# Performance work log

Hardware: AMD Instinct MI355X
Metric: run time of the kernel (lower is better)

## Reference

```python
import jax, jax.numpy as jnp
import numpy as np

B, L, D_IN, H, N, NL = 16, 5000, 12, 256, 32, 4  # N = d_state//2 complex modes


def layer_norm(x, g, b, eps=1e-5):
    m = x.mean(-1, keepdims=True)
    v = ((x - m) ** 2).mean(-1, keepdims=True)
    return (x - m) * jax.lax.rsqrt(v + eps) * g + b


def s4d_kernel(log_dt, logA_re, A_im, Cp, length):
    # S4D-style diagonal SSM kernel (ZOH discretization), conjugate-symmetric -> 2*real
    dt = jnp.exp(log_dt)                      # (H,)
    A = -jnp.exp(logA_re) + 1j * A_im         # (H, N)
    C = Cp[..., 0] + 1j * Cp[..., 1]          # (H, N)
    dtA = A * dt[:, None]                     # (H, N)
    Ct = C * (jnp.exp(dtA) - 1.0) / A         # (H, N)
    V = jnp.exp(dtA[:, :, None] * jnp.arange(length, dtype=log_dt.dtype))  # (H, N, L) Vandermonde
    return 2.0 * jnp.einsum('hn,hnl->hl', Ct, V).real  # (H, L)


def s4_block(u, log_dt, logA_re, A_im, Cp, D, W_glu, b_glu):
    # u: (B, L, H), transposed=False convention
    length = u.shape[1]
    K = s4d_kernel(log_dt, logA_re, A_im, Cp, length)     # (H, L)
    n_fft = 2 * length
    k_f = jnp.fft.rfft(K, n=n_fft)                        # (H, F)
    u_f = jnp.fft.rfft(u, n=n_fft, axis=1)                # (B, F, H)
    y = jnp.fft.irfft(u_f * k_f.T[None], n=n_fft, axis=1)[:, :length]  # causal conv
    y = y + u * D                                         # skip connection
    y = jax.nn.gelu(y)
    y = y @ W_glu + b_glu                                 # (B, L, 2H)
    return jax.nn.glu(y, axis=-1)                         # (B, L, H)


def setup_inputs() -> dict:
    key = jax.random.key(0)
    ks = jax.random.split(key, 8)
    dt_min, dt_max = 1e-3, 1e-1
    log_dt = np.log(dt_min) + jax.random.uniform(ks[2], (NL, H)) * (np.log(dt_max) - np.log(dt_min))
    A_im = jnp.broadcast_to(np.pi * jnp.arange(N, dtype=jnp.float32), (NL, H, N)).copy()
    return {
        'x': jax.random.normal(ks[0], (B, L, D_IN), jnp.float32),
        'W_in': jax.random.normal(ks[1], (D_IN, H), jnp.float32) / np.sqrt(D_IN),
        'b_in': jnp.zeros((H,), jnp.float32),
        'ln_g': jnp.ones((NL, H), jnp.float32),
        'ln_b': jnp.zeros((NL, H), jnp.float32),
        'log_dt': log_dt.astype(jnp.float32),
        'logA_re': jnp.full((NL, H, N), np.log(0.5), jnp.float32),
        'A_im': A_im,
        'Cp': jax.random.normal(ks[3], (NL, H, N, 2), jnp.float32) * (0.5 ** 0.5),
        'D': jax.random.normal(ks[4], (NL, H), jnp.float32),
        'W_glu': jax.random.normal(ks[5], (NL, H, 2 * H), jnp.float32) / np.sqrt(H),
        'b_glu': jnp.zeros((NL, 2 * H), jnp.float32),
        'fn_g': jnp.ones((H,), jnp.float32),
        'fn_b': jnp.zeros((H,), jnp.float32),
    }


def reference(x, W_in, b_in, ln_g, ln_b, log_dt, logA_re, A_im, Cp, D, W_glu, b_glu, fn_g, fn_b):
    x = x @ W_in + b_in  # (B, L, H)
    for i in range(NL):
        z = layer_norm(x, ln_g[i], ln_b[i])  # prenorm
        residual = z
        y = s4_block(z, log_dt[i], logA_re[i], A_im[i], Cp[i], D[i], W_glu[i], b_glu[i])
        x = y + residual  # dropout is identity in eval
    return layer_norm(x, fn_g, fn_b)
```

## Files before the change

### kernel.cpp

```cpp
#include <hip/hip_runtime.h>
#include <math.h>

#define BB 16
#define LL 5000
#define DIN 12
#define HH 256
#define NN 32
#define NLAYER 4
#define LC 128
#define NCH 40
#define TAIL 8
#define COLS (BB*NCH)
#define NROWS (BB*LL)
#define KU 192

typedef __attribute__((ext_vector_type(8))) _Float16 f16x8;
typedef __attribute__((ext_vector_type(4))) float f32x4;

__device__ __forceinline__ float fast_gelu(float a) {
  float z = fmaf(0.0713548163f * a, a * a, 1.5957691216f * a);
  float e = __expf(-z);
  return a * __builtin_amdgcn_rcpf(1.0f + e);
}

__device__ __forceinline__ unsigned pk2h(float a, float b) {
  union { _Float16 h[2]; unsigned u; } x;
  x.h[0] = (_Float16)a; x.h[1] = (_Float16)b;
  return x.u;
}

__device__ __forceinline__ float2 upk2(unsigned u) {
  union { unsigned u; _Float16 h[2]; } x;
  x.u = u;
  return make_float2((float)x.h[0], (float)x.h[1]);
}

__global__ __launch_bounds__(128) void paramT_kernel(
    const float* __restrict__ log_dt, const float* __restrict__ logA_re,
    const float* __restrict__ A_im, const float* __restrict__ Cp,
    const float* __restrict__ Dv, int l,
    _Float16* __restrict__ Tc, _Float16* __restrict__ V, float* __restrict__ WLc) {
  int h = blockIdx.x;
  int t = threadIdx.x;
  __shared__ float s_are[NN], s_aim[NN], s_cre[NN], s_cim[NN];
  __shared__ float s_K[128];
  if (t < NN) {
    int n = t;
    int idx = (l * HH + h) * NN + n;
    float dt = expf(log_dt[l * HH + h]);
    float Are = -expf(logA_re[idx]);
    float Aim = A_im[idx];
    float are = Are * dt, aim = Aim * dt;
    float e = expf(are);
    float wre = e * cosf(aim), wim = e * sinf(aim);
    float cr = Cp[2 * idx], ci = Cp[2 * idx + 1];
    float nre = wre - 1.0f, nim = wim;
    float tre = cr * nre - ci * nim;
    float tim = cr * nim + ci * nre;
    float inv = 1.0f / (Are * Are + Aim * Aim);
    s_are[n] = are; s_aim[n] = aim;
    s_cre[n] = 2.0f * (tre * Are + tim * Aim) * inv;
    s_cim[n] = 2.0f * (tim * Are - tre * Aim) * inv;
    float eL = expf(128.0f * are);
    float ang = 128.0f * aim;
    WLc[h * 64 + 2 * n] = eL * cosf(ang);
    WLc[h * 64 + 2 * n + 1] = eL * sinf(ang);
  }
  __syncthreads();
  {
    float ksum = 0.0f;
    unsigned* brow = (unsigned*)(Tc + ((size_t)h * 128 + t) * KU + 128);
    for (int n = 0; n < NN; n++) {
      float are = s_are[n], aim = s_aim[n];
      float cre = s_cre[n], cim = s_cim[n];
      float ft = (float)t;
      float E = expf(are * ft);
      float a = aim * ft;
      float wtre = E * cosf(a), wtim = E * sinf(a);
      ksum = fmaf(cre, wtre, ksum);
      ksum = fmaf(-cim, wtim, ksum);
      float ew = expf(are);
      float wre = ew * cosf(aim), wim = ew * sinf(aim);
      float wpre = wtre * wre - wtim * wim;
      float wpim = wtre * wim + wtim * wre;
      float bre = cre * wpre - cim * wpim;
      float bim = -(cre * wpim + cim * wpre);
      brow[n] = pk2h(bre, bim);
      float fk = (float)(127 - t);
      float E2 = expf(are * fk);
      float a2 = aim * fk;
      V[((size_t)h * 64 + 2 * n) * 128 + t] = (_Float16)(E2 * cosf(a2));
      V[((size_t)h * 64 + 2 * n + 1) * 128 + t] = (_Float16)(E2 * sinf(a2));
    }
    s_K[t] = ksum;
  }
  __syncthreads();
  float D = Dv[l * HH + h];
  unsigned* row = (unsigned*)(Tc + ((size_t)h * 128 + t) * KU);
  for (int q = 0; q < 64; q++) {
    float v0 = 0.0f, v1 = 0.0f;
    int d0 = t - 2 * q;
    int d1 = d0 - 1;
    if (d0 >= 0) v0 = s_K[d0] + (d0 == 0 ? D : 0.0f);
    if (d1 >= 0) v1 = s_K[d1] + (d1 == 0 ? D : 0.0f);
    row[q] = pk2h(v0, v1);
  }
}

__global__ __launch_bounds__(256) void wt_kernel(
    const float* __restrict__ W, _Float16* __restrict__ Wt) {
  int gid = blockIdx.x * 256 + threadIdx.x;
  int l = gid >> 9, col = gid & 511;
  const float* w = W + (size_t)l * HH * 512 + col;
  _Float16* o = Wt + (size_t)gid * HH;
  for (int k = 0; k < HH; k++) o[k] = (_Float16)(w[(size_t)k * 512]);
}

__global__ __launch_bounds__(256) void proj_kernel(
    const float* __restrict__ x, const float* __restrict__ Win,
    const float* __restrict__ bin, _Float16* __restrict__ X) {
  int tp = threadIdx.x & 127, rs = threadIdx.x >> 7;
  int h0 = 2 * tp;
  float w0[DIN], w1[DIN];
#pragma unroll
  for (int k = 0; k < DIN; k++) {
    w0[k] = Win[k * HH + h0];
    w1[k] = Win[k * HH + h0 + 1];
  }
  float b0 = bin[h0], b1 = bin[h0 + 1];
  for (int row = blockIdx.x * 2 + rs; row < NROWS; row += gridDim.x * 2) {
    float a0 = b0, a1 = b1;
#pragma unroll
    for (int k = 0; k < DIN; k++) {
      float xv = x[(size_t)row * DIN + k];
      a0 = fmaf(xv, w0[k], a0);
      a1 = fmaf(xv, w1[k], a1);
    }
    *(unsigned*)(X + (size_t)row * HH + h0) = pk2h(a0, a1);
  }
}

__global__ __launch_bounds__(256) void ln_kernel(
    const _Float16* __restrict__ in, float* __restrict__ out,
    const float* __restrict__ g, const float* __restrict__ b) {
  int wave = threadIdx.x >> 6, lane = threadIdx.x & 63;
  int row = blockIdx.x * 4 + wave;
  uint2 pv = *(const uint2*)(in + (size_t)row * HH + 4 * lane);
  float2 v01 = upk2(pv.x), v23 = upk2(pv.y);
  float s = v01.x + v01.y + v23.x + v23.y;
  float q = v01.x * v01.x + v01.y * v01.y + v23.x * v23.x + v23.y * v23.y;
#pragma unroll
  for (int m = 1; m < 64; m <<= 1) { s += __shfl_xor(s, m); q += __shfl_xor(q, m); }
  float mean = s * (1.0f / HH);
  float var = q * (1.0f / HH) - mean * mean;
  float rstd = rsqrtf(var + 1e-5f);
  float4 gg = ((const float4*)g)[lane];
  float4 bb = ((const float4*)b)[lane];
  float4 o;
  o.x = (v01.x - mean) * rstd * gg.x + bb.x;
  o.y = (v01.y - mean) * rstd * gg.y + bb.y;
  o.z = (v23.x - mean) * rstd * gg.z + bb.z;
  o.w = (v23.y - mean) * rstd * gg.w + bb.w;
  ((float4*)(out + (size_t)row * HH))[lane] = o;
}

__global__ __launch_bounds__(256) void lnU_kernel(
    _Float16* __restrict__ stream, _Float16* __restrict__ U,
    const float* __restrict__ g, const float* __restrict__ b) {
  __shared__ unsigned short Ut[64][260];
  int col = blockIdx.x;
  int bI = col / NCH, cI = col % NCH;
  int len = (cI == NCH - 1) ? TAIL : 128;
  int wave = threadIdx.x >> 6, lane = threadIdx.x & 63;
  float4 gg = ((const float4*)g)[lane];
  float4 bv = ((const float4*)b)[lane];
  size_t base = ((size_t)bI * LL + (size_t)cI * 128) * HH;
#pragma unroll
  for (int half = 0; half < 2; half++) {
    if (half) __syncthreads();
    int t0 = half * 64;
    int lenh = len - t0;
    lenh = lenh < 0 ? 0 : (lenh > 64 ? 64 : lenh);
    for (int idx = threadIdx.x; idx < (64 - lenh) * 260; idx += 256) {
      int r = idx / 260;
      Ut[lenh + r][idx - r * 260] = 0;
    }
    for (int it = 0; it < 16; it++) {
      int tl = it * 4 + wave;
      if (tl < lenh) {
        int tau = t0 + tl;
        uint2 pv = *(const uint2*)(stream + base + (size_t)tau * HH + 4 * lane);
        float2 v01 = upk2(pv.x), v23 = upk2(pv.y);
        float s = v01.x + v01.y + v23.x + v23.y;
        float q = v01.x * v01.x + v01.y * v01.y + v23.x * v23.x + v23.y * v23.y;
#pragma unroll
        for (int m = 1; m < 64; m <<= 1) { s += __shfl_xor(s, m); q += __shfl_xor(q, m); }
        float mean = s * (1.0f / HH);
        float var = q * (1.0f / HH) - mean * mean;
        float rstd = rsqrtf(var + 1e-5f);
        float o0 = (v01.x - mean) * rstd * gg.x + bv.x;
        float o1 = (v01.y - mean) * rstd * gg.y + bv.y;
        float o2 = (v23.x - mean) * rstd * gg.z + bv.z;
        float o3 = (v23.y - mean) * rstd * gg.w + bv.w;
        uint2 p;
        p.x = pk2h(o0, o1);
        p.y = pk2h(o2, o3);
        *(uint2*)(stream + base + (size_t)tau * HH + 4 * lane) = p;
        *(uint2*)&Ut[tl][4 * lane] = p;
      }
    }
    __syncthreads();
    for (int rep = 0; rep < 8; rep++) {
      int linear = rep * 256 + threadIdx.x;
      int h = linear >> 3, ub = linear & 7;
      unsigned* dst = (unsigned*)(U + ((size_t)h * COLS + col) * KU) + half * 32;
#pragma unroll
      for (int s2 = 0; s2 < 4; s2++) {
        int u = ub + s2 * 8;
        dst[u] = (unsigned)Ut[2 * u][h] | ((unsigned)Ut[2 * u + 1][h] << 16);
      }
    }
  }
}

__global__ __launch_bounds__(256) void gemmA_kernel(
    const _Float16* __restrict__ V, const _Float16* __restrict__ U,
    _Float16* __restrict__ P) {
  __shared__ _Float16 As[64 * 72];
  __shared__ _Float16 Bs[128 * 72];
  int h = blockIdx.x, c0 = blockIdx.y * 128;
  int t = threadIdx.x;
  int w = t >> 6, lane = t & 63, lr = lane & 15, quad = lane >> 4;
  int mh = w & 1, nh = w >> 1;
  f32x4 acc[2][4];
#pragma unroll
  for (int i = 0; i < 2; i++)
#pragma unroll
    for (int j = 0; j < 4; j++) acc[i][j] = (f32x4)(0.0f);

  for (int kt = 0; kt < 128; kt += 64) {
#pragma unroll
    for (int i = 0; i < 2; i++) {
      int idx = t + 256 * i;
      int m = idx >> 3, q = idx & 7;
      *(uint4*)&As[m * 72 + q * 8] =
          *(const uint4*)(V + ((size_t)h * 64 + m) * 128 + kt + q * 8);
    }
#pragma unroll
    for (int i = 0; i < 4; i++) {
      int idx = t + 256 * i;
      int jj = idx >> 3, q = idx & 7;
      *(uint4*)&Bs[jj * 72 + q * 8] =
          *(const uint4*)(U + ((size_t)h * COLS + c0 + jj) * KU + kt + q * 8);
    }
    __syncthreads();
#pragma unroll
    for (int ks = 0; ks < 2; ks++) {
      f16x8 af[2], bf[4];
#pragma unroll
      for (int i = 0; i < 2; i++)
        af[i] = *(const f16x8*)&As[(mh * 32 + i * 16 + lr) * 72 + ks * 32 + quad * 8];
#pragma unroll
      for (int j = 0; j < 4; j++)
        bf[j] = *(const f16x8*)&Bs[(nh * 64 + j * 16 + lr) * 72 + ks * 32 + quad * 8];
#pragma unroll
      for (int i = 0; i < 2; i++)
#pragma unroll
        for (int j = 0; j < 4; j++)
          acc[i][j] = __builtin_amdgcn_mfma_f32_16x16x32_f16(af[i], bf[j], acc[i][j], 0, 0, 0);
    }
    __syncthreads();
  }
#pragma unroll
  for (int i = 0; i < 2; i++) {
#pragma unroll
    for (int j = 0; j < 4; j++) {
      int n2 = mh * 32 + i * 16 + quad * 4;
      int colx = c0 + nh * 64 + j * 16 + lr;
      f32x4 a = acc[i][j];
      uint2 r;
      r.x = pk2h(a[0], a[1]);
      r.y = pk2h(a[2], a[3]);
      *(uint2*)(P + ((size_t)h * COLS + colx) * 64 + n2) = r;
    }
  }
}

__global__ __launch_bounds__(256) void combine_kernel(
    const _Float16* __restrict__ P, _Float16* __restrict__ U,
    const float* __restrict__ WLc) {
  int h = blockIdx.x >> 1;
  int bh = blockIdx.x & 1;
  int n = threadIdx.x & 31;
  int b = bh * 8 + (threadIdx.x >> 5);
  float wre = WLc[h * 64 + 2 * n], wim = WLc[h * 64 + 2 * n + 1];
  const _Float16* p = P + ((size_t)h * COLS + (size_t)b * NCH) * 64 + 2 * n;
  _Float16* u = U + ((size_t)h * COLS + (size_t)b * NCH) * KU + 128 + 2 * n;
  float cre = 0.0f, cim = 0.0f;
#pragma unroll 4
  for (int c = 0; c < NCH; c++) {
    float2 v = upk2(*(const unsigned*)(p + (size_t)c * 64));
    *(unsigned*)(u + (size_t)c * KU) = pk2h(cre, cim);
    float nre = fmaf(wre, cre, v.x) - wim * cim;
    float nim = fmaf(wre, cim, v.y) + wim * cre;
    cre = nre; cim = nim;
  }
}

__global__ __launch_bounds__(256) void gemmC_kernel(
    const _Float16* __restrict__ Tc, const _Float16* __restrict__ U,
    _Float16* __restrict__ Yt) {
  __shared__ _Float16 As[128 * 72];
  __shared__ _Float16 Bs[128 * 72];
  int h = blockIdx.x, c0 = blockIdx.y * 128;
  int t = threadIdx.x;
  int w = t >> 6, lane = t & 63, lr = lane & 15, quad = lane >> 4;
  f32x4 acc[2][8];
#pragma unroll
  for (int i = 0; i < 2; i++)
#pragma unroll
    for (int j = 0; j < 8; j++) acc[i][j] = (f32x4)(0.0f);

  for (int kt = 0; kt < KU; kt += 64) {
#pragma unroll
    for (int i = 0; i < 4; i++) {
      int idx = t + 256 * i;
      int m = idx >> 3, q = idx & 7;
      *(uint4*)&As[m * 72 + q * 8] =
          *(const uint4*)(Tc + ((size_t)h * 128 + m) * KU + kt + q * 8);
    }
#pragma unroll
    for (int i = 0; i < 4; i++) {
      int idx = t + 256 * i;
      int jj = idx >> 3, q = idx & 7;
      *(uint4*)&Bs[jj * 72 + q * 8] =
          *(const uint4*)(U + ((size_t)h * COLS + c0 + jj) * KU + kt + q * 8);
    }
    __syncthreads();
#pragma unroll
    for (int ks = 0; ks < 2; ks++) {
      f16x8 af[2], bf[8];
#pragma unroll
      for (int i = 0; i < 2; i++)
        af[i] = *(const f16x8*)&As[(w * 32 + i * 16 + lr) * 72 + ks * 32 + quad * 8];
#pragma unroll
      for (int j = 0; j < 8; j++)
        bf[j] = *(const f16x8*)&Bs[(j * 16 + lr) * 72 + ks * 32 + quad * 8];
#pragma unroll
      for (int i = 0; i < 2; i++)
#pragma unroll
        for (int j = 0; j < 8; j++)
          acc[i][j] = __builtin_amdgcn_mfma_f32_16x16x32_f16(af[i], bf[j], acc[i][j], 0, 0, 0);
    }
    __syncthreads();
  }
#pragma unroll
  for (int i = 0; i < 2; i++) {
#pragma unroll
    for (int j = 0; j < 8; j++) {
      int tb = w * 32 + i * 16 + quad * 4;
      int colx = c0 + j * 16 + lr;
      f32x4 a = acc[i][j];
      uint2 r;
      r.x = pk2h(fast_gelu(a[0]), fast_gelu(a[1]));
      r.y = pk2h(fast_gelu(a[2]), fast_gelu(a[3]));
      *(uint2*)(Yt + ((size_t)h * COLS + colx) * 128 + tb) = r;
    }
  }
}

__global__ __launch_bounds__(256) void gemm_glu_mfma(
    const _Float16* __restrict__ Yt, const _Float16* __restrict__ Wt,
    const float* __restrict__ bg, _Float16* __restrict__ Xio) {
  __shared__ uint4 smemq[2304];
  _Float16* As = (_Float16*)smemq;
  _Float16* Bs = (_Float16*)smemq + 128 * 64;
  float* gl = (float*)smemq;
  int t = threadIdx.x;
  int col = blockIdx.x;
  int bI = col / NCH, pt = col % NCH;
  int len = (pt == NCH - 1) ? TAIL : 128;
  size_t row0 = (size_t)bI * LL + (size_t)pt * 128;
  int c0 = blockIdx.y * 64;
  int w = t >> 6, lane = t & 63;
  int lr = lane & 15, quad = lane >> 4;
  int rh = w & 1, ch = w >> 1;
  int oct = lane & 15, hq = lane >> 4;
  int godd = hq & 1;
  int jbase = godd * 4;
  int goct = (oct + (oct >> 3)) & 7;
  f32x4 acc[4][4];
#pragma unroll
  for (int i = 0; i < 4; i++)
#pragma unroll
    for (int j = 0; j < 4; j++) acc[i][j] = (f32x4)(0.0f);

  int jb[4] = {ch * 32, ch * 32 + 16, 64 + ch * 32, 80 + ch * 32};

  for (int kt = 0; kt < HH; kt += 64) {
#pragma unroll
    for (int p = 0; p < 4; p++) {
      int hl = p * 16 + w * 4 + hq;
      uint4 v = *(const uint4*)(Yt + ((size_t)(kt + hl) * COLS + col) * 128 + oct * 8);
      uint4 pv;
      pv.x = __shfl_xor((int)v.x, 16);
      pv.y = __shfl_xor((int)v.y, 16);
      pv.z = __shfl_xor((int)v.z, 16);
      pv.w = __shfl_xor((int)v.w, 16);
      unsigned a0 = godd ? pv.z : v.x;
      unsigned a1 = godd ? pv.w : v.y;
      unsigned b0 = godd ? v.z : pv.x;
      unsigned b1 = godd ? v.w : pv.y;
      unsigned p0 = (a0 & 0xffffu) | (b0 << 16);
      unsigned p1 = (a0 >> 16) | (b0 & 0xffff0000u);
      unsigned p2 = (a1 & 0xffffu) | (b1 << 16);
      unsigned p3 = (a1 >> 16) | (b1 & 0xffff0000u);
      int soc = (hl >> 3) ^ goct;
      char* basep = (char*)As + oct * 1024 + (hl & 6) * 2;
      { int j = jbase;     *(unsigned*)(basep + j * 128 + ((soc ^ j) * 16)) = p0; }
      { int j = jbase + 1; *(unsigned*)(basep + j * 128 + ((soc ^ j) * 16)) = p1; }
      { int j = jbase + 2; *(unsigned*)(basep + j * 128 + ((soc ^ j) * 16)) = p2; }
      { int j = jbase + 3; *(unsigned*)(basep + j * 128 + ((soc ^ j) * 16)) = p3; }
    }
#pragma unroll
    for (int i = 0; i < 4; i++) {
      int idx = t + 256 * i;
      int jj = idx >> 3, q = idx & 7;
      int colw = (jj < 64) ? (c0 + jj) : (192 + c0 + jj);
      *(uint4*)&Bs[jj * 72 + q * 8] =
          *(const uint4*)(Wt + (size_t)colw * HH + kt + q * 8);
    }
    __syncthreads();
#pragma unroll
    for (int ks = 0; ks < 2; ks++) {
      f16x8 af[4], bf[4];
#pragma unroll
      for (int i = 0; i < 4; i++) {
        int tt = rh * 64 + i * 16 + lr;
        int ttg = tt >> 3;
        int so = (ks * 4 + quad) ^ (tt & 7) ^ ((ttg + (ttg >> 3)) & 7);
        af[i] = *(const f16x8*)((const char*)As + tt * 128 + so * 16);
      }
#pragma unroll
      for (int j = 0; j < 4; j++)
        bf[j] = *(const f16x8*)&Bs[(jb[j] + lr) * 72 + ks * 32 + quad * 8];
#pragma unroll
      for (int i = 0; i < 4; i++)
#pragma unroll
        for (int j = 0; j < 4; j++)
          acc[i][j] = __builtin_amdgcn_mfma_f32_16x16x32_f16(af[i], bf[j], acc[i][j], 0, 0, 0);
    }
    __syncthreads();
  }

#pragma unroll
  for (int i = 0; i < 4; i++) {
#pragma unroll
    for (int r = 0; r < 4; r++) {
      int rowl = rh * 64 + i * 16 + quad * 4 + r;
#pragma unroll
      for (int jp = 0; jp < 2; jp++) {
        int hl = ch * 32 + jp * 16 + lr;
        int h = c0 + hl;
        float g1 = acc[i][jp][r] + bg[h];
        float g2 = acc[i][jp + 2][r] + bg[256 + h];
        float sig = __builtin_amdgcn_rcpf(1.0f + __expf(-g2));
        gl[rowl * 68 + hl] = g1 * sig;
      }
    }
  }
  __syncthreads();

#pragma unroll
  for (int rep = 0; rep < 4; rep++) {
    int lin = rep * 256 + t;
    int rowl = lin >> 3, hc = lin & 7;
    if (rowl < len) {
      size_t row = row0 + rowl;
      int hb = c0 + hc * 8;
      uint4 zv = *(const uint4*)(Xio + row * HH + hb);
      float2 z01 = upk2(zv.x), z23 = upk2(zv.y), z45 = upk2(zv.z), z67 = upk2(zv.w);
      const float* gp = &gl[rowl * 68 + hc * 8];
      uint4 r;
      r.x = pk2h(gp[0] + z01.x, gp[1] + z01.y);
      r.y = pk2h(gp[2] + z23.x, gp[3] + z23.y);
      r.z = pk2h(gp[4] + z45.x, gp[5] + z45.y);
      r.w = pk2h(gp[6] + z67.x, gp[7] + z67.y);
      *(uint4*)(Xio + row * HH + hb) = r;
    }
  }
}

extern "C" void kernel_launch(void* const* d_in, const int* in_sizes, int n_in,
                              void* d_out, int out_size, void* d_ws, size_t ws_size,
                              hipStream_t stream) {
  const float* x      = (const float*)d_in[0];
  const float* Win    = (const float*)d_in[1];
  const float* bin    = (const float*)d_in[2];
  const float* ln_g   = (const float*)d_in[3];
  const float* ln_b   = (const float*)d_in[4];
  const float* log_dt = (const float*)d_in[5];
  const float* logA   = (const float*)d_in[6];
  const float* A_im   = (const float*)d_in[7];
  const float* Cp     = (const float*)d_in[8];
  const float* Dv     = (const float*)d_in[9];
  const float* Wglu   = (const float*)d_in[10];
  const float* bglu   = (const float*)d_in[11];
  const float* fn_g   = (const float*)d_in[12];
  const float* fn_b   = (const float*)d_in[13];
  float* out = (float*)d_out;
  float* ws = (float*)d_ws;

  _Float16* Xs = (_Float16*)ws;
  float* Pf = ws + (size_t)NROWS * HH;
  _Float16* Tc = (_Float16*)(Pf + (size_t)HH * COLS * 64);
  _Float16* V  = Tc + (size_t)HH * 128 * KU;
  _Float16* U  = V + (size_t)HH * 64 * 128;
  _Float16* Wt = U + (size_t)HH * COLS * KU;
  float* WLc = (float*)(Wt + (size_t)NLAYER * 512 * HH);
  _Float16* P16 = (_Float16*)Pf;
  _Float16* Yt  = (_Float16*)Pf;

  wt_kernel<<<(NLAYER * 512) / 256, 256, 0, stream>>>(Wglu, Wt);
  proj_kernel<<<2048, 256, 0, stream>>>(x, Win, bin, Xs);

  for (int l = 0; l < NLAYER; l++) {
    paramT_kernel<<<HH, 128, 0, stream>>>(log_dt, logA, A_im, Cp, Dv, l, Tc, V, WLc);
    lnU_kernel<<<COLS, 256, 0, stream>>>(Xs, U, ln_g + l * HH, ln_b + l * HH);
    gemmA_kernel<<<dim3(HH, COLS / 128), 256, 0, stream>>>(V, U, P16);
    combine_kernel<<<HH * 2, 256, 0, stream>>>(P16, U, WLc);
    gemmC_kernel<<<dim3(HH, COLS / 128), 256, 0, stream>>>(Tc, U, Yt);
    gemm_glu_mfma<<<dim3(COLS, 4), 256, 0, stream>>>(
        Yt, Wt + (size_t)l * 512 * HH, bglu + (size_t)l * 2 * HH, Xs);
  }
  ln_kernel<<<NROWS / 4, 256, 0, stream>>>(Xs, out, fn_g, fn_b);
}
```

Measured before the change: 901.9 us.

## Fuse chunk-state GEMM with sequential chunk combine per head and batch

```diff
diff --git a/kernel.cpp b/kernel.cpp
--- a/kernel.cpp
+++ b/kernel.cpp
@@ -223,20 +223,19 @@
   }
 }
 
-__global__ __launch_bounds__(256) void gemmA_kernel(
-    const _Float16* __restrict__ V, const _Float16* __restrict__ U,
-    _Float16* __restrict__ P) {
-  __shared__ _Float16 As[64 * 72];
-  __shared__ _Float16 Bs[128 * 72];
-  int h = blockIdx.x, c0 = blockIdx.y * 128;
+__global__ __launch_bounds__(256) void gemmAC_kernel(
+    const _Float16* __restrict__ V, _Float16* __restrict__ U,
+    const float* __restrict__ WLc) {
+  __shared__ float smf[4096];
+  _Float16* As = (_Float16*)smf;
+  _Float16* Bs = As + 64 * 72;
+  float* Ps = smf;
+  int h = blockIdx.x, b = blockIdx.y;
   int t = threadIdx.x;
   int w = t >> 6, lane = t & 63, lr = lane & 15, quad = lane >> 4;
-  int mh = w & 1, nh = w >> 1;
-  f32x4 acc[2][4];
-#pragma unroll
-  for (int i = 0; i < 2; i++)
-#pragma unroll
-    for (int j = 0; j < 4; j++) acc[i][j] = (f32x4)(0.0f);
+  f32x4 acc[3];
+#pragma unroll
+  for (int j = 0; j < 3; j++) acc[j] = (f32x4)(0.0f);
 
   for (int kt = 0; kt < 128; kt += 64) {
 #pragma unroll
@@ -247,63 +246,48 @@
           *(const uint4*)(V + ((size_t)h * 64 + m) * 128 + kt + q * 8);
     }
 #pragma unroll
-    for (int i = 0; i < 4; i++) {
+    for (int i = 0; i < 2; i++) {
       int idx = t + 256 * i;
-      int jj = idx >> 3, q = idx & 7;
-      *(uint4*)&Bs[jj * 72 + q * 8] =
-          *(const uint4*)(U + ((size_t)h * COLS + c0 + jj) * KU + kt + q * 8);
+      if (idx < 384) {
+        int jj = idx >> 3, q = idx & 7;
+        uint4 v = make_uint4(0u, 0u, 0u, 0u);
+        if (jj < NCH)
+          v = *(const uint4*)(U + ((size_t)h * COLS + (size_t)b * NCH + jj) * KU + kt + q * 8);
+        *(uint4*)&Bs[jj * 72 + q * 8] = v;
+      }
     }
     __syncthreads();
 #pragma unroll
     for (int ks = 0; ks < 2; ks++) {
-      f16x8 af[2], bf[4];
-#pragma unroll
-      for (int i = 0; i < 2; i++)
-        af[i] = *(const f16x8*)&As[(mh * 32 + i * 16 + lr) * 72 + ks * 32 + quad * 8];
-#pragma unroll
-      for (int j = 0; j < 4; j++)
-        bf[j] = *(const f16x8*)&Bs[(nh * 64 + j * 16 + lr) * 72 + ks * 32 + quad * 8];
-#pragma unroll
-      for (int i = 0; i < 2; i++)
-#pragma unroll
-        for (int j = 0; j < 4; j++)
-          acc[i][j] = __builtin_amdgcn_mfma_f32_16x16x32_f16(af[i], bf[j], acc[i][j], 0, 0, 0);
-    }
-    __syncthreads();
-  }
-#pragma unroll
-  for (int i = 0; i < 2; i++) {
-#pragma unroll
-    for (int j = 0; j < 4; j++) {
-      int n2 = mh * 32 + i * 16 + quad * 4;
-      int colx = c0 + nh * 64 + j * 16 + lr;
-      f32x4 a = acc[i][j];
-      uint2 r;
-      r.x = pk2h(a[0], a[1]);
-      r.y = pk2h(a[2], a[3]);
-      *(uint2*)(P + ((size_t)h * COLS + colx) * 64 + n2) = r;
-    }
-  }
-}
-
-__global__ __launch_bounds__(256) void combine_kernel(
-    const _Float16* __restrict__ P, _Float16* __restrict__ U,
-    const float* __restrict__ WLc) {
-  int h = blockIdx.x >> 1;
-  int bh = blockIdx.x & 1;
-  int n = threadIdx.x & 31;
-  int b = bh * 8 + (threadIdx.x >> 5);
-  float wre = WLc[h * 64 + 2 * n], wim = WLc[h * 64 + 2 * n + 1];
-  const _Float16* p = P + ((size_t)h * COLS + (size_t)b * NCH) * 64 + 2 * n;
-  _Float16* u = U + ((size_t)h * COLS + (size_t)b * NCH) * KU + 128 + 2 * n;
-  float cre = 0.0f, cim = 0.0f;
-#pragma unroll 4
-  for (int c = 0; c < NCH; c++) {
-    float2 v = upk2(*(const unsigned*)(p + (size_t)c * 64));
-    *(unsigned*)(u + (size_t)c * KU) = pk2h(cre, cim);
-    float nre = fmaf(wre, cre, v.x) - wim * cim;
-    float nim = fmaf(wre, cim, v.y) + wim * cre;
-    cre = nre; cim = nim;
+      f16x8 af = *(const f16x8*)&As[(w * 16 + lr) * 72 + ks * 32 + quad * 8];
+#pragma unroll
+      for (int j = 0; j < 3; j++) {
+        f16x8 bf = *(const f16x8*)&Bs[(j * 16 + lr) * 72 + ks * 32 + quad * 8];
+        acc[j] = __builtin_amdgcn_mfma_f32_16x16x32_f16(af, bf, acc[j], 0, 0, 0);
+      }
+    }
+    __syncthreads();
+  }
+#pragma unroll
+  for (int j = 0; j < 3; j++)
+#pragma unroll
+    for (int r = 0; r < 4; r++)
+      Ps[(w * 16 + quad * 4 + r) * 49 + j * 16 + lr] = acc[j][r];
+  __syncthreads();
+
+  if (t < 32) {
+    int n = t;
+    float wre = WLc[h * 64 + 2 * n], wim = WLc[h * 64 + 2 * n + 1];
+    float cre = 0.0f, cim = 0.0f;
+    _Float16* u = U + ((size_t)h * COLS + (size_t)b * NCH) * KU + 128 + 2 * n;
+    for (int c = 0; c < NCH; c++) {
+      float vre = Ps[(2 * n) * 49 + c];
+      float vim = Ps[(2 * n + 1) * 49 + c];
+      *(unsigned*)(u + (size_t)c * KU) = pk2h(cre, cim);
+      float nre = fmaf(wre, cre, vre) - wim * cim;
+      float nim = fmaf(wre, cim, vim) + wim * cre;
+      cre = nre; cim = nim;
+    }
   }
 }
 
@@ -518,7 +502,6 @@
   _Float16* U  = V + (size_t)HH * 64 * 128;
   _Float16* Wt = U + (size_t)HH * COLS * KU;
   float* WLc = (float*)(Wt + (size_t)NLAYER * 512 * HH);
-  _Float16* P16 = (_Float16*)Pf;
   _Float16* Yt  = (_Float16*)Pf;
 
   wt_kernel<<<(NLAYER * 512) / 256, 256, 0, stream>>>(Wglu, Wt);
@@ -527,8 +510,7 @@
   for (int l = 0; l < NLAYER; l++) {
     paramT_kernel<<<HH, 128, 0, stream>>>(log_dt, logA, A_im, Cp, Dv, l, Tc, V, WLc);
     lnU_kernel<<<COLS, 256, 0, stream>>>(Xs, U, ln_g + l * HH, ln_b + l * HH);
-    gemmA_kernel<<<dim3(HH, COLS / 128), 256, 0, stream>>>(V, U, P16);
-    combine_kernel<<<HH * 2, 256, 0, stream>>>(P16, U, WLc);
+    gemmAC_kernel<<<dim3(HH, BB), 256, 0, stream>>>(V, U, WLc);
     gemmC_kernel<<<dim3(HH, COLS / 128), 256, 0, stream>>>(Tc, U, Yt);
     gemm_glu_mfma<<<dim3(COLS, 4), 256, 0, stream>>>(
         Yt, Wt + (size_t)l * 512 * HH, bglu + (size_t)l * 2 * HH, Xs);
```

Result: faster. 875.5 us (-2.9%).
